# Kernel optimization log

Measured on AMD Instinct MI355X. Metric: run time of the kernel, lower is better.

## Reference

```python
import jax, jax.numpy as jnp
import numpy as np

EMBED_DIM = 1024
NUM_HEADS = 16
HEAD_DIM = EMBED_DIM // NUM_HEADS
B, S = 2, 2048


def setup_inputs() -> dict:
    key = jax.random.key(0)
    ks = jax.random.split(key, 9)
    d = EMBED_DIM
    scale = 1.0 / np.sqrt(d)
    inp = {
        "x": jax.random.normal(ks[0], (B, S, d), dtype=jnp.float32),
        "mask": jnp.ones((B, S), dtype=jnp.int32),
        "Wq": jax.random.normal(ks[1], (d, d), dtype=jnp.float32) * scale,
        "bq": jnp.zeros((d,), dtype=jnp.float32),
        "Wk": jax.random.normal(ks[2], (d, d), dtype=jnp.float32) * scale,
        "bk": jnp.zeros((d,), dtype=jnp.float32),
        "Wv": jax.random.normal(ks[3], (d, d), dtype=jnp.float32) * scale,
        "bv": jnp.zeros((d,), dtype=jnp.float32),
        "Wo": jax.random.normal(ks[4], (d, d), dtype=jnp.float32) * scale,
        "bo": jnp.zeros((d,), dtype=jnp.float32),
    }
    return inp


def reference(x, mask, Wq, bq, Wk, bk, Wv, bv, Wo, bo):
    b, s, _ = x.shape
    # projections; torch Linear computes x @ W.T + b
    q = (x @ Wq.T + bq).reshape(b, s, NUM_HEADS, HEAD_DIM).transpose(0, 2, 1, 3)
    k = (x @ Wk.T + bk).reshape(b, s, NUM_HEADS, HEAD_DIM).transpose(0, 2, 1, 3)
    v = (x @ Wv.T + bv).reshape(b, s, NUM_HEADS, HEAD_DIM).transpose(0, 2, 1, 3)
    scores = jnp.einsum("bhqd,bhkd->bhqk", q, k) / np.sqrt(HEAD_DIM)  # (B,H,S,S)
    m = (mask == 0)[:, None, None, :]  # broadcast over heads and query pos
    scores = jnp.where(m, jnp.float32(-1e9), scores)
    attn = jax.nn.softmax(scores, axis=-1)
    out = jnp.einsum("bhqk,bhkd->bhqd", attn, v)
    out = out.transpose(0, 2, 1, 3).reshape(b, s, EMBED_DIM)
    return out @ Wo.T + bo
```

## Files before the change

kernel.cpp:

```cpp
#include <hip/hip_runtime.h>

#define EMBED 1024
#define NHEAD 16
#define HDIM  64
#define BB    2
#define SS    2048

typedef __bf16 bf16x8 __attribute__((ext_vector_type(8)));
typedef float  f32x4  __attribute__((ext_vector_type(4)));
typedef _Float16 f16x8 __attribute__((ext_vector_type(8)));
typedef __fp16 hf16x2 __attribute__((ext_vector_type(2)));

#if defined(__has_builtin)
#if __has_builtin(__builtin_amdgcn_exp2f)
#define EXP2(x) __builtin_amdgcn_exp2f(x)
#else
#define EXP2(x) exp2f(x)
#endif
#else
#define EXP2(x) exp2f(x)
#endif

__device__ __forceinline__ unsigned short f2bf(float f) {
  union { float f; unsigned u; } v; v.f = f;
  unsigned r = v.u + 0x7fffu + ((v.u >> 16) & 1u);
  return (unsigned short)(r >> 16);
}

__device__ __forceinline__ float bf2f(unsigned short u) {
  union { unsigned u; float f; } v; v.u = ((unsigned)u) << 16;
  return v.f;
}

__device__ __forceinline__ unsigned short f2h(float f) {
  union { _Float16 h; unsigned short u; } t;
  t.h = (_Float16)f;
  return t.u;
}

__device__ __forceinline__ void g2l16(const unsigned short* g, unsigned short* l) {
  __builtin_amdgcn_global_load_lds(
      (const __attribute__((address_space(1))) unsigned int*)g,
      (__attribute__((address_space(3))) unsigned int*)l, 16, 0, 0);
}

__global__ __launch_bounds__(256)
void cvt5_kernel(const float* __restrict__ x,  const float* __restrict__ Wq,
                 const float* __restrict__ Wk, const float* __restrict__ Wv,
                 const float* __restrict__ Wo, const int* __restrict__ mask,
                 unsigned short* __restrict__ xb,  unsigned short* __restrict__ Wqb,
                 unsigned short* __restrict__ Wkb, unsigned short* __restrict__ Wvb,
                 unsigned short* __restrict__ Wob, float* __restrict__ mbias) {
  const int i = blockIdx.x * 256 + threadIdx.x;
  if (i < (1 << 21)) {
    const float* src;
    unsigned short* dst;
    int j;
    if (i < (1 << 20)) {
      src = x; dst = xb; j = i;
    } else {
      const int t = i - (1 << 20);
      const int r = t >> 18;
      j = t & ((1 << 18) - 1);
      src = (r == 0) ? Wq : (r == 1) ? Wk : (r == 2) ? Wv : Wo;
      dst = (r == 0) ? Wqb : (r == 1) ? Wkb : (r == 2) ? Wvb : Wob;
    }
    const float4 f = ((const float4*)src)[j];
    ushort4 u;
    u.x = f2bf(f.x); u.y = f2bf(f.y); u.z = f2bf(f.z); u.w = f2bf(f.w);
    ((ushort4*)dst)[j] = u;
  } else {
    const int j = i - (1 << 21);
    const int4 m = ((const int4*)mask)[j];
    float4 o;
    o.x = m.x ? 0.f : -1e30f; o.y = m.y ? 0.f : -1e30f;
    o.z = m.z ? 0.f : -1e30f; o.w = m.w ? 0.f : -1e30f;
    ((float4*)mbias)[j] = o;
  }
}

template <typename EpiFn>
__device__ __forceinline__
void gemm_core(const unsigned short* __restrict__ A,
               const unsigned short* __restrict__ Bm,
               int m0, int n0, EpiFn epi) {
  __shared__ unsigned short sA[128 * 64];
  __shared__ unsigned short sB[128 * 64];
  const int tid = threadIdx.x;
  const int l  = tid & 63;
  const int w  = tid >> 6;
  const int lm = l & 15;
  const int qd = l >> 4;
  const int wm = w & 1;
  const int wn = w >> 1;

  f32x4 acc[4][4];
#pragma unroll
  for (int i = 0; i < 4; ++i)
#pragma unroll
    for (int j = 0; j < 4; ++j) acc[i][j] = (f32x4){0.f, 0.f, 0.f, 0.f};

  for (int k0 = 0; k0 < EMBED; k0 += 64) {
#pragma unroll
    for (int i = 0; i < 4; ++i) {
      const int t = i * 256 + tid;
      const int r = t >> 3;
      const int c = (t & 7) ^ (r & 7);
      g2l16(A + (m0 + r) * EMBED + k0 + c * 8, &sA[(i * 256 + (w << 6)) * 8]);
      g2l16(Bm + (n0 + r) * EMBED + k0 + c * 8, &sB[(i * 256 + (w << 6)) * 8]);
    }
    __syncthreads();
#pragma unroll
    for (int kk = 0; kk < 2; ++kk) {
      bf16x8 af[4], bfr[4];
#pragma unroll
      for (int mi = 0; mi < 4; ++mi) {
        const int R = wm * 64 + mi * 16 + lm;
        const int ch = R * 8 + (((kk << 2) + qd) ^ (R & 7));
        af[mi] = *(const bf16x8*)&sA[ch * 8];
      }
#pragma unroll
      for (int ni = 0; ni < 4; ++ni) {
        const int R = wn * 64 + ni * 16 + lm;
        const int ch = R * 8 + (((kk << 2) + qd) ^ (R & 7));
        bfr[ni] = *(const bf16x8*)&sB[ch * 8];
      }
#pragma unroll
      for (int mi = 0; mi < 4; ++mi)
#pragma unroll
        for (int ni = 0; ni < 4; ++ni)
          acc[mi][ni] = __builtin_amdgcn_mfma_f32_16x16x32_bf16(
              af[mi], bfr[ni], acc[mi][ni], 0, 0, 0);
    }
    __syncthreads();
  }

#pragma unroll
  for (int mi = 0; mi < 4; ++mi)
#pragma unroll
    for (int ni = 0; ni < 4; ++ni) {
      const int mb = m0 + wm * 64 + mi * 16 + qd * 4;
      const int n  = n0 + wn * 64 + ni * 16 + lm;
      epi(acc[mi][ni], mb, n);
    }
}

__device__ __forceinline__ void decode_tile(int flat, int& a0, int& b0) {
  const int sub = flat & 15;
  const int g = flat >> 4;
  a0 = ((g >> 2) * 2 + (sub >> 3));
  b0 = ((g & 3) * 8 + (sub & 7));
}

__global__ __launch_bounds__(256)
void gemm_qkv(const unsigned short* __restrict__ xb,
              const unsigned short* __restrict__ Wqb,
              const unsigned short* __restrict__ Wkb,
              const unsigned short* __restrict__ Wvb,
              const float* __restrict__ bq, const float* __restrict__ bk,
              const float* __restrict__ bv,
              unsigned short* __restrict__ Qb, unsigned short* __restrict__ Kb,
              unsigned short* __restrict__ VTb) {
  const int z = blockIdx.y;
  int a0, b0;
  decode_tile(blockIdx.x, a0, b0);
  if (z < 2) {
    const unsigned short* A = z ? Wkb : Wqb;
    const float* bias = z ? bk : bq;
    unsigned short* O = z ? Kb : Qb;
    const float scale = z ? 1.0f : 0.125f * 1.4426950408889634f;
    gemm_core(A, xb, a0 * 128, b0 * 128, [&](const f32x4& v, int mb, int n) {
      const float4 bvv = *(const float4*)&bias[mb];
      const int h = mb >> 6, d0 = mb & 63;
      const int b = n >> 11, s = n & 2047;
      int sw = s;
      if (z == 1)
        sw = (s & ~31) | (((s >> 2) & 1) << 4) | (((s >> 3) & 3) << 2) | (s & 3);
      ushort4 u;
      u.x = f2bf((v.x + bvv.x) * scale); u.y = f2bf((v.y + bvv.y) * scale);
      u.z = f2bf((v.z + bvv.z) * scale); u.w = f2bf((v.w + bvv.w) * scale);
      *(ushort4*)&O[(((b * NHEAD + h) * SS) + sw) * HDIM + d0] = u;
    });
  } else {
    gemm_core(xb, Wvb, b0 * 128, a0 * 128, [&](const f32x4& v, int mb, int n) {
      const float bvv = bv[n];
      const int b = mb >> 11, s = mb & 2047;
      const int h = n >> 6, d = n & 63;
      ushort4 u;
      u.x = f2h(v.x + bvv); u.y = f2h(v.y + bvv);
      u.z = f2h(v.z + bvv); u.w = f2h(v.w + bvv);
      *(ushort4*)&VTb[(((b * NHEAD + h) * HDIM) + d) * SS + s] = u;
    });
  }
}

__global__ __launch_bounds__(256)
void gemm_out(const unsigned short* __restrict__ Wob,
              const unsigned short* __restrict__ Ob,
              const float* __restrict__ bo, float* __restrict__ out) {
  int a0, b0;
  decode_tile(blockIdx.x, a0, b0);
  gemm_core(Wob, Ob, a0 * 128, b0 * 128, [&](const f32x4& v, int mb, int n) {
    const float4 bvv = *(const float4*)&bo[mb];
    float4 o;
    o.x = v.x + bvv.x; o.y = v.y + bvv.y; o.z = v.z + bvv.z; o.w = v.w + bvv.w;
    *(float4*)&out[n * EMBED + mb] = o;
  });
}

__global__ __launch_bounds__(256)
void attn_kernel(const unsigned short* __restrict__ Q,
                 const unsigned short* __restrict__ K,
                 const unsigned short* __restrict__ VT,
                 const float* __restrict__ mbias,
                 unsigned short* __restrict__ Opart,
                 float* __restrict__ Lpart) {
  __shared__ unsigned short sK[2][64 * 64];
  __shared__ unsigned short sV[2][64 * 64];
  __shared__ float sMB[SS / 2];
  const int tid = threadIdx.x;
  const int l = tid & 63, w = tid >> 6;
  const int lm = l & 15, qd = l >> 4;
  const int b = blockIdx.z & 1, sp = blockIdx.z >> 1, h = blockIdx.y;
  const int q0 = blockIdx.x * 128 + w * 32;
  const unsigned short* Qh = Q + ((b * NHEAD + h) * SS) * HDIM;
  const unsigned short* Kh = K + ((b * NHEAD + h) * SS) * HDIM;
  const unsigned short* Vh = VT + ((b * NHEAD + h) * HDIM) * SS;
  const float* mb = mbias + b * SS + sp * (SS / 2);
  unsigned short* Op = Opart + sp * (BB * SS * EMBED);
  float* Lp = Lpart + sp * (BB * NHEAD * SS);
  const int kb0 = sp * (SS / 2);

  bf16x8 qf[2][2];
#pragma unroll
  for (int g = 0; g < 2; ++g) {
    qf[g][0] = *(const bf16x8*)&Qh[(q0 + g * 16 + lm) * HDIM + qd * 8];
    qf[g][1] = *(const bf16x8*)&Qh[(q0 + g * 16 + lm) * HDIM + 32 + qd * 8];
  }

  auto stageKV = [&](int buf, int kb) {
#pragma unroll
    for (int i = 0; i < 2; ++i) {
      const int t = i * 256 + tid;
      const int r = t >> 3;
      const int c = (t & 7) ^ (r & 7);
      g2l16(Kh + (kb + r) * HDIM + c * 8, &sK[buf][(i * 256 + (w << 6)) * 8]);
      g2l16(Vh + r * SS + kb + c * 8, &sV[buf][(i * 256 + (w << 6)) * 8]);
    }
  };

  g2l16((const unsigned short*)(mb + tid * 4), (unsigned short*)&sMB[w * 256]);
  stageKV(0, kb0);

  f32x4 Od[2][4];
#pragma unroll
  for (int g = 0; g < 2; ++g)
#pragma unroll
    for (int i = 0; i < 4; ++i) Od[g][i] = (f32x4){0.f, 0.f, 0.f, 0.f};
  float lsum[2] = {0.f, 0.f};

  __syncthreads();

  const int NT = (SS / 2) / 64;
  for (int t = 0; t < NT; ++t) {
    const int curb = t & 1;
    if (t + 1 < NT) stageKV(curb ^ 1, kb0 + (t + 1) * 64);

    f16x8 pf8[2][2];
#pragma unroll
    for (int p = 0; p < 2; ++p) {
      union PK { hf16x2 h2[4]; f16x8 v; } pk0, pk1;
#pragma unroll
      for (int jj = 0; jj < 2; ++jj) {
        const int j = p * 2 + jj;
        const int R = j * 16 + lm;
        const bf16x8 k0 = *(const bf16x8*)&sK[curb][(R * 8 + (qd ^ (lm & 7))) * 8];
        const bf16x8 k1 = *(const bf16x8*)&sK[curb][(R * 8 + ((4 + qd) ^ (lm & 7))) * 8];
        const float4 bj = *(const float4*)&sMB[t * 64 + p * 32 + qd * 8 + jj * 4];
        const f32x4 binit = (f32x4){bj.x, bj.y, bj.z, bj.w};
#pragma unroll
        for (int g = 0; g < 2; ++g) {
          f32x4 t0 = binit;
          t0 = __builtin_amdgcn_mfma_f32_16x16x32_bf16(k0, qf[g][0], t0, 0, 0, 0);
          t0 = __builtin_amdgcn_mfma_f32_16x16x32_bf16(k1, qf[g][1], t0, 0, 0, 0);
          const float p0 = EXP2(t0[0]);
          const float p1 = EXP2(t0[1]);
          const float p2 = EXP2(t0[2]);
          const float p3 = EXP2(t0[3]);
          lsum[g] += (p0 + p1) + (p2 + p3);
          const hf16x2 lo = __builtin_amdgcn_cvt_pkrtz(p0, p1);
          const hf16x2 hi = __builtin_amdgcn_cvt_pkrtz(p2, p3);
          if (g == 0) { pk0.h2[jj * 2] = lo; pk0.h2[jj * 2 + 1] = hi; }
          else        { pk1.h2[jj * 2] = lo; pk1.h2[jj * 2 + 1] = hi; }
        }
      }
      pf8[0][p] = pk0.v;
      pf8[1][p] = pk1.v;
    }

#pragma unroll
    for (int dt = 0; dt < 4; ++dt) {
      const int row = dt * 16 + lm;
#pragma unroll
      for (int p = 0; p < 2; ++p) {
        const f16x8 vf =
            *(const f16x8*)&sV[curb][row * 64 + ((p * 4 + qd) ^ (lm & 7)) * 8];
        Od[0][dt] = __builtin_amdgcn_mfma_f32_16x16x32_f16(vf, pf8[0][p],
                                                           Od[0][dt], 0, 0, 0);
        Od[1][dt] = __builtin_amdgcn_mfma_f32_16x16x32_f16(vf, pf8[1][p],
                                                           Od[1][dt], 0, 0, 0);
      }
    }
    __syncthreads();
  }

#pragma unroll
  for (int g = 0; g < 2; ++g) {
    float ls = lsum[g];
    ls += __shfl_xor(ls, 16);
    ls += __shfl_xor(ls, 32);
    if (qd == 0) Lp[(b * NHEAD + h) * SS + q0 + g * 16 + lm] = ls;
#pragma unroll
    for (int dt = 0; dt < 4; ++dt) {
      ushort4 u;
      u.x = f2bf(Od[g][dt][0]); u.y = f2bf(Od[g][dt][1]);
      u.z = f2bf(Od[g][dt][2]); u.w = f2bf(Od[g][dt][3]);
      *(ushort4*)&Op[(b * SS + q0 + g * 16 + lm) * EMBED + h * HDIM +
                     dt * 16 + qd * 4] = u;
    }
  }
}

__global__ __launch_bounds__(256)
void combine_kernel(const unsigned short* __restrict__ Opart,
                    const float* __restrict__ Lpart,
                    unsigned short* __restrict__ Ob) {
  const int i = blockIdx.x * 256 + threadIdx.x;
  const int base = i * 8;
  const int token = base >> 10;
  const int h = (base >> 6) & 15;
  const int b = token >> 11, q = token & 2047;
  const int lidx = (b * NHEAD + h) * SS + q;
  const float ls = Lpart[lidx] + Lpart[BB * NHEAD * SS + lidx];
  const float rinv = 1.f / ls;
  const ushort4* p0 = (const ushort4*)&Opart[base];
  const ushort4* p1 = (const ushort4*)&Opart[BB * SS * EMBED + base];
  ushort4 o[2];
#pragma unroll
  for (int k = 0; k < 2; ++k) {
    const ushort4 a = p0[k], c = p1[k];
    o[k].x = f2bf((bf2f(a.x) + bf2f(c.x)) * rinv);
    o[k].y = f2bf((bf2f(a.y) + bf2f(c.y)) * rinv);
    o[k].z = f2bf((bf2f(a.z) + bf2f(c.z)) * rinv);
    o[k].w = f2bf((bf2f(a.w) + bf2f(c.w)) * rinv);
  }
  *(ushort4*)&Ob[base] = o[0];
  *(ushort4*)&Ob[base + 4] = o[1];
}

extern "C" void kernel_launch(void* const* d_in, const int* in_sizes, int n_in,
                              void* d_out, int out_size, void* d_ws, size_t ws_size,
                              hipStream_t stream) {
  const float* x  = (const float*)d_in[0];
  const int* mask = (const int*)d_in[1];
  const float* Wq = (const float*)d_in[2];
  const float* bq = (const float*)d_in[3];
  const float* Wk = (const float*)d_in[4];
  const float* bk = (const float*)d_in[5];
  const float* Wv = (const float*)d_in[6];
  const float* bv = (const float*)d_in[7];
  const float* Wo = (const float*)d_in[8];
  const float* bo = (const float*)d_in[9];
  float* out = (float*)d_out;

  char* ws = (char*)d_ws;
  const size_t MB = 1024 * 1024;
  unsigned short* xb  = (unsigned short*)(ws);
  unsigned short* Ob  = (unsigned short*)(ws);
  unsigned short* Wqb = (unsigned short*)(ws + 8 * MB);
  unsigned short* Wkb = Wqb + 1024 * 1024;
  unsigned short* Wvb = Wkb + 1024 * 1024;
  unsigned short* Wob = Wvb + 1024 * 1024;
  unsigned short* Qb  = (unsigned short*)(ws + 16 * MB);
  unsigned short* Kb  = (unsigned short*)(ws + 24 * MB);
  unsigned short* VTb = (unsigned short*)(ws + 32 * MB);
  unsigned short* Opart = (unsigned short*)(ws + 40 * MB);
  float* mbb   = (float*)(ws + 56 * MB);
  float* Lpart = (float*)(ws + 56 * MB + 64 * 1024);

  cvt5_kernel<<<8196, 256, 0, stream>>>(x, Wq, Wk, Wv, Wo, mask,
                                        xb, Wqb, Wkb, Wvb, Wob, mbb);
  gemm_qkv<<<dim3(256, 3), 256, 0, stream>>>(xb, Wqb, Wkb, Wvb, bq, bk, bv,
                                             Qb, Kb, VTb);
  attn_kernel<<<dim3(16, 16, 4), 256, 0, stream>>>(Qb, Kb, VTb, mbb,
                                                   Opart, Lpart);
  combine_kernel<<<2048, 256, 0, stream>>>(Opart, Lpart, Ob);
  gemm_out<<<256, 256, 0, stream>>>(Wob, Ob, bo, out);
}
```

Before: 215.9 us.

## Shrink attention tiles to 16 queries per wave, single-buffer KV, raise occupancy

The attention kernel now gives each wave 16 query rows instead of 32 and launches twice as many blocks. It drops the double-buffered K/V shared-memory staging in favour of load-then-sync each tile, and sets launch bounds to 8 blocks per CU to cut register and LDS use. It also adds s_setprio around the MFMA groups and interleaves the PV MFMAs per p-chunk. The aim is higher occupancy and latency hiding across waves. The cost is that each K/V tile is now reused by half as many queries, so total K/V LDS traffic doubles, and prefetch overlap within a block is lost.

```diff
diff --git a/kernel.cpp b/kernel.cpp
--- a/kernel.cpp
+++ b/kernel.cpp
@@ -208,21 +208,21 @@
   });
 }
 
-__global__ __launch_bounds__(256)
+__global__ __launch_bounds__(256, 8)
 void attn_kernel(const unsigned short* __restrict__ Q,
                  const unsigned short* __restrict__ K,
                  const unsigned short* __restrict__ VT,
                  const float* __restrict__ mbias,
                  unsigned short* __restrict__ Opart,
                  float* __restrict__ Lpart) {
-  __shared__ unsigned short sK[2][64 * 64];
-  __shared__ unsigned short sV[2][64 * 64];
+  __shared__ unsigned short sK[64 * 64];
+  __shared__ unsigned short sV[64 * 64];
   __shared__ float sMB[SS / 2];
   const int tid = threadIdx.x;
   const int l = tid & 63, w = tid >> 6;
   const int lm = l & 15, qd = l >> 4;
   const int b = blockIdx.z & 1, sp = blockIdx.z >> 1, h = blockIdx.y;
-  const int q0 = blockIdx.x * 128 + w * 32;
+  const int q0 = blockIdx.x * 64 + w * 16;
   const unsigned short* Qh = Q + ((b * NHEAD + h) * SS) * HDIM;
   const unsigned short* Kh = K + ((b * NHEAD + h) * SS) * HDIM;
   const unsigned short* Vh = VT + ((b * NHEAD + h) * HDIM) * SS;
@@ -231,103 +231,79 @@
   float* Lp = Lpart + sp * (BB * NHEAD * SS);
   const int kb0 = sp * (SS / 2);
 
-  bf16x8 qf[2][2];
-#pragma unroll
-  for (int g = 0; g < 2; ++g) {
-    qf[g][0] = *(const bf16x8*)&Qh[(q0 + g * 16 + lm) * HDIM + qd * 8];
-    qf[g][1] = *(const bf16x8*)&Qh[(q0 + g * 16 + lm) * HDIM + 32 + qd * 8];
-  }
-
-  auto stageKV = [&](int buf, int kb) {
+  bf16x8 qf[2];
+  qf[0] = *(const bf16x8*)&Qh[(q0 + lm) * HDIM + qd * 8];
+  qf[1] = *(const bf16x8*)&Qh[(q0 + lm) * HDIM + 32 + qd * 8];
+
+  auto stageKV = [&](int kb) {
 #pragma unroll
     for (int i = 0; i < 2; ++i) {
       const int t = i * 256 + tid;
       const int r = t >> 3;
       const int c = (t & 7) ^ (r & 7);
-      g2l16(Kh + (kb + r) * HDIM + c * 8, &sK[buf][(i * 256 + (w << 6)) * 8]);
-      g2l16(Vh + r * SS + kb + c * 8, &sV[buf][(i * 256 + (w << 6)) * 8]);
+      g2l16(Kh + (kb + r) * HDIM + c * 8, &sK[(i * 256 + (w << 6)) * 8]);
+      g2l16(Vh + r * SS + kb + c * 8, &sV[(i * 256 + (w << 6)) * 8]);
     }
   };
 
   g2l16((const unsigned short*)(mb + tid * 4), (unsigned short*)&sMB[w * 256]);
-  stageKV(0, kb0);
-
-  f32x4 Od[2][4];
-#pragma unroll
-  for (int g = 0; g < 2; ++g)
-#pragma unroll
-    for (int i = 0; i < 4; ++i) Od[g][i] = (f32x4){0.f, 0.f, 0.f, 0.f};
-  float lsum[2] = {0.f, 0.f};
-
-  __syncthreads();
+
+  f32x4 Od[4];
+#pragma unroll
+  for (int i = 0; i < 4; ++i) Od[i] = (f32x4){0.f, 0.f, 0.f, 0.f};
+  float lsum = 0.f;
 
   const int NT = (SS / 2) / 64;
   for (int t = 0; t < NT; ++t) {
-    const int curb = t & 1;
-    if (t + 1 < NT) stageKV(curb ^ 1, kb0 + (t + 1) * 64);
-
-    f16x8 pf8[2][2];
+    stageKV(kb0 + t * 64);
+    __syncthreads();
+
 #pragma unroll
     for (int p = 0; p < 2; ++p) {
-      union PK { hf16x2 h2[4]; f16x8 v; } pk0, pk1;
+      union PK { hf16x2 h2[4]; f16x8 v; } pk;
 #pragma unroll
       for (int jj = 0; jj < 2; ++jj) {
         const int j = p * 2 + jj;
         const int R = j * 16 + lm;
-        const bf16x8 k0 = *(const bf16x8*)&sK[curb][(R * 8 + (qd ^ (lm & 7))) * 8];
-        const bf16x8 k1 = *(const bf16x8*)&sK[curb][(R * 8 + ((4 + qd) ^ (lm & 7))) * 8];
+        const bf16x8 k0 = *(const bf16x8*)&sK[(R * 8 + (qd ^ (lm & 7))) * 8];
+        const bf16x8 k1 = *(const bf16x8*)&sK[(R * 8 + ((4 + qd) ^ (lm & 7))) * 8];
         const float4 bj = *(const float4*)&sMB[t * 64 + p * 32 + qd * 8 + jj * 4];
-        const f32x4 binit = (f32x4){bj.x, bj.y, bj.z, bj.w};
-#pragma unroll
-        for (int g = 0; g < 2; ++g) {
-          f32x4 t0 = binit;
-          t0 = __builtin_amdgcn_mfma_f32_16x16x32_bf16(k0, qf[g][0], t0, 0, 0, 0);
-          t0 = __builtin_amdgcn_mfma_f32_16x16x32_bf16(k1, qf[g][1], t0, 0, 0, 0);
-          const float p0 = EXP2(t0[0]);
-          const float p1 = EXP2(t0[1]);
-          const float p2 = EXP2(t0[2]);
-          const float p3 = EXP2(t0[3]);
-          lsum[g] += (p0 + p1) + (p2 + p3);
-          const hf16x2 lo = __builtin_amdgcn_cvt_pkrtz(p0, p1);
-          const hf16x2 hi = __builtin_amdgcn_cvt_pkrtz(p2, p3);
-          if (g == 0) { pk0.h2[jj * 2] = lo; pk0.h2[jj * 2 + 1] = hi; }
-          else        { pk1.h2[jj * 2] = lo; pk1.h2[jj * 2 + 1] = hi; }
-        }
+        f32x4 t0 = (f32x4){bj.x, bj.y, bj.z, bj.w};
+        __builtin_amdgcn_s_setprio(1);
+        t0 = __builtin_amdgcn_mfma_f32_16x16x32_bf16(k0, qf[0], t0, 0, 0, 0);
+        t0 = __builtin_amdgcn_mfma_f32_16x16x32_bf16(k1, qf[1], t0, 0, 0, 0);
+        __builtin_amdgcn_s_setprio(0);
+        const float p0 = EXP2(t0[0]);
+        const float p1 = EXP2(t0[1]);
+        const float p2 = EXP2(t0[2]);
+        const float p3 = EXP2(t0[3]);
+        lsum += (p0 + p1) + (p2 + p3);
+        pk.h2[jj * 2] = __builtin_amdgcn_cvt_pkrtz(p0, p1);
+        pk.h2[jj * 2 + 1] = __builtin_amdgcn_cvt_pkrtz(p2, p3);
       }
-      pf8[0][p] = pk0.v;
-      pf8[1][p] = pk1.v;
-    }
-
-#pragma unroll
-    for (int dt = 0; dt < 4; ++dt) {
-      const int row = dt * 16 + lm;
-#pragma unroll
-      for (int p = 0; p < 2; ++p) {
+      const f16x8 pf8 = pk.v;
+      __builtin_amdgcn_s_setprio(1);
+#pragma unroll
+      for (int dt = 0; dt < 4; ++dt) {
         const f16x8 vf =
-            *(const f16x8*)&sV[curb][row * 64 + ((p * 4 + qd) ^ (lm & 7)) * 8];
-        Od[0][dt] = __builtin_amdgcn_mfma_f32_16x16x32_f16(vf, pf8[0][p],
-                                                           Od[0][dt], 0, 0, 0);
-        Od[1][dt] = __builtin_amdgcn_mfma_f32_16x16x32_f16(vf, pf8[1][p],
-                                                           Od[1][dt], 0, 0, 0);
+            *(const f16x8*)&sV[(dt * 16 + lm) * 64 + ((p * 4 + qd) ^ (lm & 7)) * 8];
+        Od[dt] = __builtin_amdgcn_mfma_f32_16x16x32_f16(vf, pf8, Od[dt], 0, 0, 0);
       }
+      __builtin_amdgcn_s_setprio(0);
     }
     __syncthreads();
   }
 
-#pragma unroll
-  for (int g = 0; g < 2; ++g) {
-    float ls = lsum[g];
-    ls += __shfl_xor(ls, 16);
-    ls += __shfl_xor(ls, 32);
-    if (qd == 0) Lp[(b * NHEAD + h) * SS + q0 + g * 16 + lm] = ls;
-#pragma unroll
-    for (int dt = 0; dt < 4; ++dt) {
-      ushort4 u;
-      u.x = f2bf(Od[g][dt][0]); u.y = f2bf(Od[g][dt][1]);
-      u.z = f2bf(Od[g][dt][2]); u.w = f2bf(Od[g][dt][3]);
-      *(ushort4*)&Op[(b * SS + q0 + g * 16 + lm) * EMBED + h * HDIM +
-                     dt * 16 + qd * 4] = u;
-    }
+  float ls = lsum;
+  ls += __shfl_xor(ls, 16);
+  ls += __shfl_xor(ls, 32);
+  if (qd == 0) Lp[(b * NHEAD + h) * SS + q0 + lm] = ls;
+#pragma unroll
+  for (int dt = 0; dt < 4; ++dt) {
+    ushort4 u;
+    u.x = f2bf(Od[dt][0]); u.y = f2bf(Od[dt][1]);
+    u.z = f2bf(Od[dt][2]); u.w = f2bf(Od[dt][3]);
+    *(ushort4*)&Op[(b * SS + q0 + lm) * EMBED + h * HDIM + dt * 16 + qd * 4] = u;
   }
 }
 
@@ -392,7 +368,7 @@
                                         xb, Wqb, Wkb, Wvb, Wob, mbb);
   gemm_qkv<<<dim3(256, 3), 256, 0, stream>>>(xb, Wqb, Wkb, Wvb, bq, bk, bv,
                                              Qb, Kb, VTb);
-  attn_kernel<<<dim3(16, 16, 4), 256, 0, stream>>>(Qb, Kb, VTb, mbb,
+  attn_kernel<<<dim3(32, 16, 4), 256, 0, stream>>>(Qb, Kb, VTb, mbb,
                                                    Opart, Lpart);
   combine_kernel<<<2048, 256, 0, stream>>>(Opart, Lpart, Ob);
   gemm_out<<<256, 256, 0, stream>>>(Wob, Ob, bo, out);
```

Measured after the change: 220.0 us. No clear change (+1.9%).

## Shrink attention blocks to two waves, single-buffer KV, interleave PV with setprio

Applied to the files above, without the earlier changes.

Attention blocks now have 128 threads covering 64 queries, launched on twice as many blocks. The double-buffered K/V staging is replaced by a single buffer with a sync after each load, which halves LDS use so more blocks can be resident. The PV MFMAs are interleaved into the per-p softmax loop, and s_setprio raises wave priority around the MFMA sections. This gives up the prefetch overlap inside a block and hopes cross-block occupancy hides load latency instead, while each K/V tile is now reloaded by twice as many blocks.

```diff
diff --git a/kernel.cpp b/kernel.cpp
--- a/kernel.cpp
+++ b/kernel.cpp
@@ -208,21 +208,21 @@
   });
 }
 
-__global__ __launch_bounds__(256)
+__global__ __launch_bounds__(128)
 void attn_kernel(const unsigned short* __restrict__ Q,
                  const unsigned short* __restrict__ K,
                  const unsigned short* __restrict__ VT,
                  const float* __restrict__ mbias,
                  unsigned short* __restrict__ Opart,
                  float* __restrict__ Lpart) {
-  __shared__ unsigned short sK[2][64 * 64];
-  __shared__ unsigned short sV[2][64 * 64];
+  __shared__ unsigned short sK[64 * 64];
+  __shared__ unsigned short sV[64 * 64];
   __shared__ float sMB[SS / 2];
   const int tid = threadIdx.x;
   const int l = tid & 63, w = tid >> 6;
   const int lm = l & 15, qd = l >> 4;
   const int b = blockIdx.z & 1, sp = blockIdx.z >> 1, h = blockIdx.y;
-  const int q0 = blockIdx.x * 128 + w * 32;
+  const int q0 = blockIdx.x * 64 + w * 32;
   const unsigned short* Qh = Q + ((b * NHEAD + h) * SS) * HDIM;
   const unsigned short* Kh = K + ((b * NHEAD + h) * SS) * HDIM;
   const unsigned short* Vh = VT + ((b * NHEAD + h) * HDIM) * SS;
@@ -238,19 +238,21 @@
     qf[g][1] = *(const bf16x8*)&Qh[(q0 + g * 16 + lm) * HDIM + 32 + qd * 8];
   }
 
-  auto stageKV = [&](int buf, int kb) {
-#pragma unroll
-    for (int i = 0; i < 2; ++i) {
-      const int t = i * 256 + tid;
+  auto stageKV = [&](int kb) {
+#pragma unroll
+    for (int i = 0; i < 4; ++i) {
+      const int t = i * 128 + tid;
       const int r = t >> 3;
       const int c = (t & 7) ^ (r & 7);
-      g2l16(Kh + (kb + r) * HDIM + c * 8, &sK[buf][(i * 256 + (w << 6)) * 8]);
-      g2l16(Vh + r * SS + kb + c * 8, &sV[buf][(i * 256 + (w << 6)) * 8]);
+      g2l16(Kh + (kb + r) * HDIM + c * 8, &sK[(i * 128 + (w << 6)) * 8]);
+      g2l16(Vh + r * SS + kb + c * 8, &sV[(i * 128 + (w << 6)) * 8]);
     }
   };
 
-  g2l16((const unsigned short*)(mb + tid * 4), (unsigned short*)&sMB[w * 256]);
-  stageKV(0, kb0);
+#pragma unroll
+  for (int j = 0; j < 2; ++j)
+    g2l16((const unsigned short*)(mb + (j * 128 + tid) * 4),
+          (unsigned short*)&sMB[(j * 2 + w) * 256]);
 
   f32x4 Od[2][4];
 #pragma unroll
@@ -259,14 +261,11 @@
     for (int i = 0; i < 4; ++i) Od[g][i] = (f32x4){0.f, 0.f, 0.f, 0.f};
   float lsum[2] = {0.f, 0.f};
 
-  __syncthreads();
-
   const int NT = (SS / 2) / 64;
   for (int t = 0; t < NT; ++t) {
-    const int curb = t & 1;
-    if (t + 1 < NT) stageKV(curb ^ 1, kb0 + (t + 1) * 64);
-
-    f16x8 pf8[2][2];
+    stageKV(kb0 + t * 64);
+    __syncthreads();
+
 #pragma unroll
     for (int p = 0; p < 2; ++p) {
       union PK { hf16x2 h2[4]; f16x8 v; } pk0, pk1;
@@ -274,15 +273,17 @@
       for (int jj = 0; jj < 2; ++jj) {
         const int j = p * 2 + jj;
         const int R = j * 16 + lm;
-        const bf16x8 k0 = *(const bf16x8*)&sK[curb][(R * 8 + (qd ^ (lm & 7))) * 8];
-        const bf16x8 k1 = *(const bf16x8*)&sK[curb][(R * 8 + ((4 + qd) ^ (lm & 7))) * 8];
+        const bf16x8 k0 = *(const bf16x8*)&sK[(R * 8 + (qd ^ (lm & 7))) * 8];
+        const bf16x8 k1 = *(const bf16x8*)&sK[(R * 8 + ((4 + qd) ^ (lm & 7))) * 8];
         const float4 bj = *(const float4*)&sMB[t * 64 + p * 32 + qd * 8 + jj * 4];
         const f32x4 binit = (f32x4){bj.x, bj.y, bj.z, bj.w};
 #pragma unroll
         for (int g = 0; g < 2; ++g) {
           f32x4 t0 = binit;
+          __builtin_amdgcn_s_setprio(1);
           t0 = __builtin_amdgcn_mfma_f32_16x16x32_bf16(k0, qf[g][0], t0, 0, 0, 0);
           t0 = __builtin_amdgcn_mfma_f32_16x16x32_bf16(k1, qf[g][1], t0, 0, 0, 0);
+          __builtin_amdgcn_s_setprio(0);
           const float p0 = EXP2(t0[0]);
           const float p1 = EXP2(t0[1]);
           const float p2 = EXP2(t0[2]);
@@ -294,22 +295,17 @@
           else        { pk1.h2[jj * 2] = lo; pk1.h2[jj * 2 + 1] = hi; }
         }
       }
-      pf8[0][p] = pk0.v;
-      pf8[1][p] = pk1.v;
-    }
-
-#pragma unroll
-    for (int dt = 0; dt < 4; ++dt) {
-      const int row = dt * 16 + lm;
-#pragma unroll
-      for (int p = 0; p < 2; ++p) {
+      const f16x8 pf0 = pk0.v;
+      const f16x8 pf1 = pk1.v;
+      __builtin_amdgcn_s_setprio(1);
+#pragma unroll
+      for (int dt = 0; dt < 4; ++dt) {
         const f16x8 vf =
-            *(const f16x8*)&sV[curb][row * 64 + ((p * 4 + qd) ^ (lm & 7)) * 8];
-        Od[0][dt] = __builtin_amdgcn_mfma_f32_16x16x32_f16(vf, pf8[0][p],
-                                                           Od[0][dt], 0, 0, 0);
-        Od[1][dt] = __builtin_amdgcn_mfma_f32_16x16x32_f16(vf, pf8[1][p],
-                                                           Od[1][dt], 0, 0, 0);
+            *(const f16x8*)&sV[(dt * 16 + lm) * 64 + ((p * 4 + qd) ^ (lm & 7)) * 8];
+        Od[0][dt] = __builtin_amdgcn_mfma_f32_16x16x32_f16(vf, pf0, Od[0][dt], 0, 0, 0);
+        Od[1][dt] = __builtin_amdgcn_mfma_f32_16x16x32_f16(vf, pf1, Od[1][dt], 0, 0, 0);
       }
+      __builtin_amdgcn_s_setprio(0);
     }
     __syncthreads();
   }
@@ -392,7 +388,7 @@
                                         xb, Wqb, Wkb, Wvb, Wob, mbb);
   gemm_qkv<<<dim3(256, 3), 256, 0, stream>>>(xb, Wqb, Wkb, Wvb, bq, bk, bv,
                                              Qb, Kb, VTb);
-  attn_kernel<<<dim3(16, 16, 4), 256, 0, stream>>>(Qb, Kb, VTb, mbb,
+  attn_kernel<<<dim3(32, 16, 4), 128, 0, stream>>>(Qb, Kb, VTb, mbb,
                                                    Opart, Lpart);
   combine_kernel<<<2048, 256, 0, stream>>>(Opart, Lpart, Ob);
   gemm_out<<<256, 256, 0, stream>>>(Wob, Ob, bo, out);
```

Result: slower. 222.9 us (+3.2%).
